# Optimization experiments

Measured on AMD Instinct MI355X. Metric: run time of the kernel, lower is better.

The kernel has to match this reference:

```python
import jax, jax.numpy as jnp
import numpy as np

N, E, DIN, DOUT, DE = 100000, 250000, 32, 32, 13


def setup_inputs() -> dict:
    key = jax.random.key(0)
    ks = jax.random.split(key, 10)
    def u(k, shape, fan):
        b = 1.0 / np.sqrt(fan)
        return jax.random.uniform(k, shape, jnp.float32, -b, b)
    x = jax.random.normal(ks[0], (N, DIN), jnp.float32)
    edge_index = jax.random.randint(ks[1], (2, E), 0, N)
    edge_attr = jax.random.uniform(ks[2], (E, DE), jnp.float32)
    # NNConv's edge network: Linear(DE -> DIN*DOUT)
    nn_w = u(ks[3], (DIN * DOUT, DE), DE)
    nn_b = u(ks[4], (DIN * DOUT,), DE)
    # NNConv root weight + bias
    root = u(ks[5], (DIN, DOUT), DIN)
    bias = jnp.zeros((DOUT,), jnp.float32)
    # GRU(input=DIN, hidden=DOUT), single layer, seq_len=1
    w_ih = u(ks[6], (3 * DOUT, DIN), DOUT)
    w_hh = u(ks[7], (3 * DOUT, DOUT), DOUT)
    b_ih = u(ks[8], (3 * DOUT,), DOUT)
    b_hh = u(ks[9], (3 * DOUT,), DOUT)
    return dict(x=x, edge_attr=edge_attr, nn_w=nn_w, nn_b=nn_b, root=root,
                bias=bias, w_ih=w_ih, w_hh=w_hh, b_ih=b_ih, b_hh=b_hh,
                edge_index=edge_index)


def reference(x, edge_attr, nn_w, nn_b, root, bias, w_ih, w_hh, b_ih, b_hh, edge_index):
    identity = x
    h0 = x  # h is None -> h = x.unsqueeze(0); squeeze the seq dim here
    # norm='_None' (identity) and Dropout in eval mode (identity)
    src, dst = edge_index[0], edge_index[1]
    # NNConv: per-edge weight matrix from edge_attr  [E, DIN, DOUT]
    W = (edge_attr @ nn_w.T + nn_b).reshape(E, DIN, DOUT)
    msg = jnp.einsum('ei,eio->eo', x[src], W)           # [E, DOUT]
    agg = jax.ops.segment_sum(msg, dst, num_segments=N)  # [N, DOUT]
    cnt = jax.ops.segment_sum(jnp.ones((E, 1), x.dtype), dst, num_segments=N)
    mean = agg / jnp.maximum(cnt, 1.0)                   # aggr='mean'
    conv = mean + x @ root + bias
    # celu then GRU step (seq_len=1)
    c = jax.nn.celu(conv)
    gi = c @ w_ih.T + b_ih
    gh = h0 @ w_hh.T + b_hh
    ir, iz, ic = jnp.split(gi, 3, axis=1)
    hr, hz, hc = jnp.split(gh, 3, axis=1)
    r = jax.nn.sigmoid(ir + hr)
    z = jax.nn.sigmoid(iz + hz)
    n = jnp.tanh(ic + r * hc)
    h_new = (1.0 - z) * n + z * h0
    out = jax.nn.relu(h_new + identity)  # res=True, act=ReLU
    return out, h_new[None]
```

## Files before the change

### kernel.cpp

```cpp
#include <hip/hip_runtime.h>
#include <hip/hip_bf16.h>
#include <stdint.h>

#define DIN 32
#define DOUT 32
#define DE 13

typedef float f32x4 __attribute__((ext_vector_type(4)));
typedef short s16x8 __attribute__((ext_vector_type(8)));
typedef int   i32x4 __attribute__((ext_vector_type(4)));
typedef unsigned int u32x4 __attribute__((ext_vector_type(4)));

__device__ __forceinline__ float bf2f(unsigned short u) {
    return __uint_as_float(((uint32_t)u) << 16);
}
__device__ __forceinline__ unsigned short f2bf(float f) {
    uint32_t b = __float_as_uint(f);
    b += 0x7FFFu + ((b >> 16) & 1u);
    return (unsigned short)(b >> 16);
}
__device__ __forceinline__ uint32_t pk2(float a, float b) {
    float2 t; t.x = a; t.y = b;
    __hip_bfloat162 h = __float22bfloat162_rn(t);
    return *(uint32_t*)&h;
}
__device__ __forceinline__ float sigm(float v) { return 1.f / (1.f + __expf(-v)); }
__device__ __forceinline__ float tanh_fast(float v) { return 2.f / (1.f + __expf(-2.f * v)) - 1.f; }


__global__ __launch_bounds__(256) void kH(const int* __restrict__ ei,
                                          int* __restrict__ cntI, int E) {
    int e = blockIdx.x * 256 + threadIdx.x;
    if (e < E) atomicAdd(&cntI[ei[E + e]], 1);
}

__global__ __launch_bounds__(1024) void kA(const int* __restrict__ cntI,
        int* __restrict__ base, float* __restrict__ degF,
        unsigned int* __restrict__ gtot, int N) {
    __shared__ int wsum[16];
    __shared__ unsigned int bbase;
    const int tid = threadIdx.x;
    const int lane = tid & 63;
    const int wv = tid >> 6;
    const int n = blockIdx.x * 1024 + tid;
    int d = (n < N) ? cntI[n] : 0;
    int sc = d;
    #pragma unroll
    for (int o = 1; o < 64; o <<= 1) {
        int t = __shfl_up(sc, o, 64);
        if (lane >= o) sc += t;
    }
    if (lane == 63) wsum[wv] = sc;
    __syncthreads();
    if (tid == 0) {
        int tot = 0;
        #pragma unroll
        for (int w = 0; w < 16; ++w) { int t = wsum[w]; wsum[w] = tot; tot += t; }
        bbase = atomicAdd(gtot, (unsigned int)tot);
    }
    __syncthreads();
    if (n < N) {
        base[n] = (int)bbase + wsum[wv] + (sc - d);
        degF[n] = (float)d;
    }
}

#define KE_LDS (28 * 512)
__global__ __launch_bounds__(256, 4) void kE(const float* __restrict__ x,
        const float* __restrict__ ea, const int* __restrict__ ei,
        const float* __restrict__ nn_w, const float* __restrict__ nn_b,
        uint32_t* __restrict__ msg, const int* __restrict__ base,
        int* __restrict__ cntI, int E) {
    __shared__ unsigned short Al[KE_LDS];
    __shared__ uint32_t trD[4][2][256];
    const int tid = threadIdx.x;
    for (int t = tid; t < KE_LDS; t += 256) {
        int j = t & 7;
        int lane = (t >> 3) & 63;
        int tile = t >> 9;
        int at2 = tile >= 14 ? 1 : 0;
        int kt = tile - at2 * 14;
        int o = at2 * 16 + (lane & 15);
        int i = ((lane >> 4) << 3) + j;
        float v = (kt < 13) ? nn_w[(i * 32 + o) * 13 + kt] : nn_b[i * 32 + o];
        Al[t] = f2bf(v);
    }
    __syncthreads();
    const int lane = tid & 63;
    const int wv = tid >> 6;
    const int el = lane & 15;
    const int quad = lane >> 4;
    const int q8 = quad << 3;
    const int wave = (blockIdx.x * 256 + tid) >> 6;
    const int nw = (gridDim.x * 256) >> 6;
    const int nstrips = E >> 4;
    int sC = wave;
    if (sC >= nstrips) return;
    int sN = sC + nw, sNN = sN + nw;

    const int eC = (sC << 4) + el;
    const int srcC = ei[eC];
    const int dstC = ei[E + eC];
    int srcN = 0, dstN = 0;
    if (sN < nstrips) {
        const int e1 = (sN << 4) + el;
        srcN = ei[e1];
        dstN = ei[E + e1];
    }
    {
        const float* eab = ea + (size_t)(sC << 4) * 13;
        #pragma unroll
        for (int t = 0; t < 4; ++t) {
            int idx = t * 64 + lane;
            if (idx < 208) trD[wv][0][idx] = __float_as_uint(eab[idx]);
        }
    }
    uint32_t eaR[4] = {0u, 0u, 0u, 0u};
    if (sN < nstrips) {
        const float* eab = ea + (size_t)(sN << 4) * 13;
        #pragma unroll
        for (int t = 0; t < 4; ++t) {
            int idx = t * 64 + lane;
            eaR[t] = (idx < 208) ? __float_as_uint(eab[idx]) : 0u;
        }
    }
    const float* xq0 = x + (size_t)srcC * 32 + q8;
    f32x4 xlo = *(const f32x4*)xq0;
    f32x4 xhi = *(const f32x4*)(xq0 + 4);
    int posC = 0;
    if (lane < 16)
        posC = base[dstC] + atomicSub(&cntI[dstC], 1) - 1;

    int pb = 0;
    const f32x4 zz = {0.f, 0.f, 0.f, 0.f};
    for (;;) {
        const bool hasN  = sN  < nstrips;
        const bool hasNN = sNN < nstrips;
        int srcNN = 0, dstNN = 0;
        if (hasNN) {
            const int e2 = (sNN << 4) + el;
            srcNN = ei[e2];
            dstNN = ei[E + e2];
        }
        if (hasN) {
            #pragma unroll
            for (int t = 0; t < 4; ++t) {
                int idx = t * 64 + lane;
                if (idx < 208) trD[wv][pb ^ 1][idx] = eaR[t];
            }
        }
        if (hasNN) {
            const float* eab = ea + (size_t)(sNN << 4) * 13;
            #pragma unroll
            for (int t = 0; t < 4; ++t) {
                int idx = t * 64 + lane;
                eaR[t] = (idx < 208) ? __float_as_uint(eab[idx]) : 0u;
            }
        }
        int posN = 0;
        if (hasN && lane < 16)
            posN = base[dstN] + atomicSub(&cntI[dstN], 1) - 1;
        i32x4 bi;
        bi[0] = pk2(xlo[0], xlo[1]);
        bi[1] = pk2(xlo[2], xlo[3]);
        bi[2] = pk2(xhi[0], xhi[1]);
        bi[3] = pk2(xhi[2], xhi[3]);
        s16x8 bfr = __builtin_bit_cast(s16x8, bi);
        s16x8 aB0 = *(const s16x8*)&Al[13 * 512 + lane * 8];
        s16x8 aB1 = *(const s16x8*)&Al[27 * 512 + lane * 8];
        f32x4 acc0 = __builtin_amdgcn_mfma_f32_16x16x32_bf16(aB0, bfr, zz, 0, 0, 0);
        f32x4 acc1 = __builtin_amdgcn_mfma_f32_16x16x32_bf16(aB1, bfr, zz, 0, 0, 0);
        #pragma unroll
        for (int kt = 0; kt < 13; ++kt) {
            s16x8 a0 = *(const s16x8*)&Al[kt * 512 + lane * 8];
            s16x8 a1 = *(const s16x8*)&Al[(14 + kt) * 512 + lane * 8];
            f32x4 y0 = __builtin_amdgcn_mfma_f32_16x16x32_bf16(a0, bfr, zz, 0, 0, 0);
            f32x4 y1 = __builtin_amdgcn_mfma_f32_16x16x32_bf16(a1, bfr, zz, 0, 0, 0);
            float gk = __uint_as_float(trD[wv][pb][el * 13 + kt]);
            #pragma unroll
            for (int r = 0; r < 4; ++r) {
                acc0[r] = fmaf(gk, y0[r], acc0[r]);
                acc1[r] = fmaf(gk, y1[r], acc1[r]);
            }
        }
        {
            u32x4 pw;
            pw[0] = pk2(acc0[0], acc1[0]);
            pw[1] = pk2(acc0[1], acc1[1]);
            pw[2] = pk2(acc0[2], acc1[2]);
            pw[3] = pk2(acc0[3], acc1[3]);
            *(u32x4*)&trD[wv][pb][el * 16 + quad * 4] = pw;
        }
        uint32_t v4s[4];
        int pp[4];
        #pragma unroll
        for (int p = 0; p < 4; ++p) {
            int e4 = (p << 2) + quad;
            v4s[p] = trD[wv][pb][e4 * 16 + el];
            pp[p] = __shfl(posC, e4, 64);
        }
        if (hasN) {
            const float* xq = x + (size_t)srcN * 32 + q8;
            xlo = *(const f32x4*)xq;
            xhi = *(const f32x4*)(xq + 4);
        }
        __builtin_amdgcn_sched_barrier(0);
        #pragma unroll
        for (int p = 0; p < 4; ++p)
            msg[(size_t)pp[p] * 16 + el] = v4s[p];
        __builtin_amdgcn_sched_barrier(0);
        if (!hasN) break;
        sC = sN; sN = sNN; sNN += nw;
        srcN = srcNN; dstN = dstNN;
        posC = posN;
        pb ^= 1;
    }
}

__global__ __launch_bounds__(256, 4) void kF(const float* __restrict__ x,
        const uint32_t* __restrict__ msg, const int* __restrict__ base,
        const float* __restrict__ degF,
        const float* __restrict__ root, const float* __restrict__ bias,
        const float* __restrict__ w_ih, const float* __restrict__ w_hh,
        const float* __restrict__ b_ih, const float* __restrict__ b_hh,
        float* __restrict__ out, float* __restrict__ hnew, int N) {
    __shared__ __align__(16) char smem[30720];
    unsigned short* Bl = (unsigned short*)smem;
    float* scr = (float*)(smem + 14336);
    unsigned short* clds = (unsigned short*)(smem + 14336);
    const int tid = threadIdx.x;
    {
        *(f32x4*)&scr[tid * 4] = *(const f32x4*)&root[tid * 4];
        #pragma unroll
        for (int it = 0; it < 3; ++it)
            *(f32x4*)&scr[1024 + it * 1024 + tid * 4] =
                *(const f32x4*)&w_hh[it * 1024 + tid * 4];
    }
    __syncthreads();
    for (int t = tid; t < 8 * 512; t += 256) {
        int j = t & 7;
        int ln = (t >> 3) & 63;
        int tt = t >> 9;
        int i = ((ln >> 4) << 3) + j;
        int c = ln & 15;
        int col = tt * 16 + c;
        float v = (col < 32) ? scr[i * 32 + col] : scr[1024 + (col - 32) * 32 + i];
        Bl[t] = f2bf(v);
    }
    __syncthreads();
    #pragma unroll
    for (int it = 0; it < 3; ++it)
        *(f32x4*)&scr[it * 1024 + tid * 4] = *(const f32x4*)&w_ih[it * 1024 + tid * 4];
    __syncthreads();
    for (int t = tid + 8 * 512; t < 14 * 512; t += 256) {
        int j = t & 7;
        int ln = (t >> 3) & 63;
        int tt = t >> 9;
        int i = ((ln >> 4) << 3) + j;
        int c = ln & 15;
        Bl[t] = f2bf(scr[((tt - 8) * 16 + c) * 32 + i]);
    }
    __syncthreads();
    const int lane = tid & 63;
    const int wv = tid >> 6;
    const int c15 = lane & 15;
    const int rowb = (lane >> 4) << 2;
    unsigned short* cl = clds + wv * 512;
    float binit[14];
    #pragma unroll
    for (int t = 0; t < 2; ++t) binit[t] = bias[t * 16 + c15];
    #pragma unroll
    for (int t = 2; t < 8; ++t) binit[t] = b_hh[t * 16 + c15 - 32];
    #pragma unroll
    for (int u = 0; u < 6; ++u) binit[8 + u] = b_ih[u * 16 + c15];
    int wave = (blockIdx.x * 256 + tid) >> 6;
    const int nw = (gridDim.x * 256) >> 6;
    const int nstrips = N >> 4;
    for (int s = wave; s < nstrips; s += nw) {
        const int n0 = s << 4;
        const float* xp = x + (size_t)(n0 + c15) * 32 + ((lane >> 4) << 3);
        f32x4 x0 = *(const f32x4*)xp;
        f32x4 x1 = *(const f32x4*)(xp + 4);
        int bs[4]; float dg[4]; float xr[4][2], ag[4][2];
        #pragma unroll
        for (int r = 0; r < 4; ++r) {
            const int n = n0 + rowb + r;
            bs[r] = base[n];
            dg[r] = degF[n];
            xr[r][0] = x[(size_t)n * 32 + c15];
            xr[r][1] = x[(size_t)n * 32 + 16 + c15];
        }
        #pragma unroll
        for (int r = 0; r < 4; ++r) {
            float a0 = 0.f, a1 = 0.f;
            const int dgi = (int)dg[r];
            const uint32_t* mp = msg + (size_t)bs[r] * 16 + c15;
            for (int j = 0; j < dgi; ++j) {
                uint32_t w = mp[j * 16];
                a0 += bf2f((unsigned short)(w & 0xFFFFu));
                a1 += bf2f((unsigned short)(w >> 16));
            }
            ag[r][0] = a0; ag[r][1] = a1;
        }
        s16x8 a;
        a[0] = (short)f2bf(x0[0]); a[1] = (short)f2bf(x0[1]);
        a[2] = (short)f2bf(x0[2]); a[3] = (short)f2bf(x0[3]);
        a[4] = (short)f2bf(x1[0]); a[5] = (short)f2bf(x1[1]);
        a[6] = (short)f2bf(x1[2]); a[7] = (short)f2bf(x1[3]);
        f32x4 D[8];
        #pragma unroll
        for (int t = 0; t < 8; ++t) {
            s16x8 b = *(const s16x8*)&Bl[(t * 64 + lane) * 8];
            f32x4 ci = {binit[t], binit[t], binit[t], binit[t]};
            D[t] = __builtin_amdgcn_mfma_f32_16x16x32_bf16(a, b, ci, 0, 0, 0);
        }
        #pragma unroll
        for (int r = 0; r < 4; ++r) {
            float icn = 1.f / fmaxf(dg[r], 1.f);
            #pragma unroll
            for (int t = 0; t < 2; ++t) {
                float conv = ag[r][t] * icn + D[t][r];
                float cv = conv > 0.f ? conv : (__expf(conv) - 1.f);
                cl[(rowb + r) * 32 + t * 16 + c15] = f2bf(cv);
            }
        }
        s16x8 a2 = *(const s16x8*)&cl[c15 * 32 + ((lane >> 4) << 3)];
        f32x4 G[6];
        #pragma unroll
        for (int u = 0; u < 6; ++u) {
            s16x8 b = *(const s16x8*)&Bl[((8 + u) * 64 + lane) * 8];
            f32x4 ci = {binit[8 + u], binit[8 + u], binit[8 + u], binit[8 + u]};
            G[u] = __builtin_amdgcn_mfma_f32_16x16x32_bf16(a2, b, ci, 0, 0, 0);
        }
        #pragma unroll
        for (int t = 0; t < 2; ++t) {
            #pragma unroll
            for (int r = 0; r < 4; ++r) {
                float rg = sigm(G[t][r] + D[2 + t][r]);
                float z  = sigm(G[2 + t][r] + D[4 + t][r]);
                float nn = tanh_fast(G[4 + t][r] + rg * D[6 + t][r]);
                float h  = (1.f - z) * nn + z * xr[r][t];
                float ov = h + xr[r][t];
                size_t oi = (size_t)(n0 + rowb + r) * 32 + t * 16 + c15;
                out[oi]  = ov > 0.f ? ov : 0.f;
                hnew[oi] = h;
            }
        }
    }
}

extern "C" void kernel_launch(void* const* d_in, const int* in_sizes, int n_in,
                              void* d_out, int out_size, void* d_ws, size_t ws_size,
                              hipStream_t stream) {
    const float* x    = (const float*)d_in[0];
    const float* ea   = (const float*)d_in[1];
    const float* nn_w = (const float*)d_in[2];
    const float* nn_b = (const float*)d_in[3];
    const float* root = (const float*)d_in[4];
    const float* bias = (const float*)d_in[5];
    const float* w_ih = (const float*)d_in[6];
    const float* w_hh = (const float*)d_in[7];
    const float* b_ih = (const float*)d_in[8];
    const float* b_hh = (const float*)d_in[9];
    const int*   ei   = (const int*)d_in[10];
    const int N = in_sizes[0] / DIN;
    const int E = in_sizes[10] / 2;
    float* out  = (float*)d_out;
    float* hnew = out + (size_t)N * DOUT;

    uint32_t* msg  = (uint32_t*)d_ws;
    char* p1 = (char*)d_ws + (size_t)E * 64;
    int*   base = (int*)p1;
    float* degF = (float*)(p1 + (size_t)N * 4);
    int*   cntI = (int*)(p1 + (size_t)N * 8);
    unsigned int* gtot = (unsigned int*)(p1 + (size_t)N * 12);

    hipMemsetAsync(cntI, 0, (size_t)N * 4 + 4, stream);
    kH<<<(E + 255) / 256, 256, 0, stream>>>(ei, cntI, E);
    kA<<<(N + 1023) / 1024, 1024, 0, stream>>>(cntI, base, degF, gtot, N);
    kE<<<1024, 256, 0, stream>>>(x, ea, ei, nn_w, nn_b, msg, base, cntI, E);
    kF<<<1024, 256, 0, stream>>>(x, msg, base, degF, root, bias,
                                 w_ih, w_hh, b_ih, b_hh, out, hnew, N);
}
```

Before: 171.2 us.

## Enlarge edge-kernel blocks and interleave per-row message gathers in node kernel

The edge kernel now runs 1024-thread blocks (512 blocks) instead of 256-thread blocks, so the 28KB bf16 weight tile in LDS is built once per 16 waves rather than per 4, cutting redundant global loads and conversion work. The node kernel's aggregation loop now walks all four rows together up to the maximum degree with predicated loads, giving more independent memory requests in flight. The x loads for the residual are also deferred until after the MFMAs. The trade-offs are extra wasted loads for low-degree rows, a larger LDS footprint per block that may limit occupancy, and higher register pressure from the interleaved gather.

```diff
diff --git a/kernel.cpp b/kernel.cpp
--- a/kernel.cpp
+++ b/kernel.cpp
@@ -66,15 +66,15 @@
 }
 
 #define KE_LDS (28 * 512)
-__global__ __launch_bounds__(256, 4) void kE(const float* __restrict__ x,
+__global__ __launch_bounds__(1024, 8) void kE(const float* __restrict__ x,
         const float* __restrict__ ea, const int* __restrict__ ei,
         const float* __restrict__ nn_w, const float* __restrict__ nn_b,
         uint32_t* __restrict__ msg, const int* __restrict__ base,
         int* __restrict__ cntI, int E) {
     __shared__ unsigned short Al[KE_LDS];
-    __shared__ uint32_t trD[4][2][256];
+    __shared__ uint32_t trD[16][2][256];
     const int tid = threadIdx.x;
-    for (int t = tid; t < KE_LDS; t += 256) {
+    for (int t = tid; t < KE_LDS; t += 1024) {
         int j = t & 7;
         int lane = (t >> 3) & 63;
         int tile = t >> 9;
@@ -91,8 +91,8 @@
     const int el = lane & 15;
     const int quad = lane >> 4;
     const int q8 = quad << 3;
-    const int wave = (blockIdx.x * 256 + tid) >> 6;
-    const int nw = (gridDim.x * 256) >> 6;
+    const int wave = (blockIdx.x * 1024 + tid) >> 6;
+    const int nw = (gridDim.x * 1024) >> 6;
     const int nstrips = E >> 4;
     int sC = wave;
     if (sC >= nstrips) return;
@@ -278,30 +278,31 @@
     const int nstrips = N >> 4;
     for (int s = wave; s < nstrips; s += nw) {
         const int n0 = s << 4;
-        const float* xp = x + (size_t)(n0 + c15) * 32 + ((lane >> 4) << 3);
-        f32x4 x0 = *(const f32x4*)xp;
-        f32x4 x1 = *(const f32x4*)(xp + 4);
-        int bs[4]; float dg[4]; float xr[4][2], ag[4][2];
+        int bs[4]; float dg[4]; int di[4];
         #pragma unroll
         for (int r = 0; r < 4; ++r) {
             const int n = n0 + rowb + r;
             bs[r] = base[n];
             dg[r] = degF[n];
-            xr[r][0] = x[(size_t)n * 32 + c15];
-            xr[r][1] = x[(size_t)n * 32 + 16 + c15];
-        }
-        #pragma unroll
-        for (int r = 0; r < 4; ++r) {
-            float a0 = 0.f, a1 = 0.f;
-            const int dgi = (int)dg[r];
-            const uint32_t* mp = msg + (size_t)bs[r] * 16 + c15;
-            for (int j = 0; j < dgi; ++j) {
-                uint32_t w = mp[j * 16];
-                a0 += bf2f((unsigned short)(w & 0xFFFFu));
-                a1 += bf2f((unsigned short)(w >> 16));
-            }
-            ag[r][0] = a0; ag[r][1] = a1;
-        }
+            di[r] = (int)dg[r];
+        }
+        int dmax = di[0];
+        #pragma unroll
+        for (int r = 1; r < 4; ++r) dmax = di[r] > dmax ? di[r] : dmax;
+        float a0[4] = {0.f, 0.f, 0.f, 0.f}, a1[4] = {0.f, 0.f, 0.f, 0.f};
+        for (int j = 0; j < dmax; ++j) {
+            #pragma unroll
+            for (int r = 0; r < 4; ++r) {
+                int jj = j < di[r] ? j : 0;
+                uint32_t w = msg[(size_t)(bs[r] + jj) * 16 + c15];
+                bool p = j < di[r];
+                a0[r] += p ? bf2f((unsigned short)(w & 0xFFFFu)) : 0.f;
+                a1[r] += p ? bf2f((unsigned short)(w >> 16)) : 0.f;
+            }
+        }
+        const float* xp = x + (size_t)(n0 + c15) * 32 + ((lane >> 4) << 3);
+        f32x4 x0 = *(const f32x4*)xp;
+        f32x4 x1 = *(const f32x4*)(xp + 4);
         s16x8 a;
         a[0] = (short)f2bf(x0[0]); a[1] = (short)f2bf(x0[1]);
         a[2] = (short)f2bf(x0[2]); a[3] = (short)f2bf(x0[3]);
@@ -317,12 +318,12 @@
         #pragma unroll
         for (int r = 0; r < 4; ++r) {
             float icn = 1.f / fmaxf(dg[r], 1.f);
-            #pragma unroll
-            for (int t = 0; t < 2; ++t) {
-                float conv = ag[r][t] * icn + D[t][r];
-                float cv = conv > 0.f ? conv : (__expf(conv) - 1.f);
-                cl[(rowb + r) * 32 + t * 16 + c15] = f2bf(cv);
-            }
+            float conv0 = a0[r] * icn + D[0][r];
+            float conv1 = a1[r] * icn + D[1][r];
+            float cv0 = conv0 > 0.f ? conv0 : (__expf(conv0) - 1.f);
+            float cv1 = conv1 > 0.f ? conv1 : (__expf(conv1) - 1.f);
+            cl[(rowb + r) * 32 + c15] = f2bf(cv0);
+            cl[(rowb + r) * 32 + 16 + c15] = f2bf(cv1);
         }
         s16x8 a2 = *(const s16x8*)&cl[c15 * 32 + ((lane >> 4) << 3)];
         f32x4 G[6];
@@ -331,6 +332,13 @@
             s16x8 b = *(const s16x8*)&Bl[((8 + u) * 64 + lane) * 8];
             f32x4 ci = {binit[8 + u], binit[8 + u], binit[8 + u], binit[8 + u]};
             G[u] = __builtin_amdgcn_mfma_f32_16x16x32_bf16(a2, b, ci, 0, 0, 0);
+        }
+        float xr[4][2];
+        #pragma unroll
+        for (int r = 0; r < 4; ++r) {
+            const int n = n0 + rowb + r;
+            xr[r][0] = x[(size_t)n * 32 + c15];
+            xr[r][1] = x[(size_t)n * 32 + 16 + c15];
         }
         #pragma unroll
         for (int t = 0; t < 2; ++t) {
@@ -378,7 +386,7 @@
     hipMemsetAsync(cntI, 0, (size_t)N * 4 + 4, stream);
     kH<<<(E + 255) / 256, 256, 0, stream>>>(ei, cntI, E);
     kA<<<(N + 1023) / 1024, 1024, 0, stream>>>(cntI, base, degF, gtot, N);
-    kE<<<1024, 256, 0, stream>>>(x, ea, ei, nn_w, nn_b, msg, base, cntI, E);
+    kE<<<512, 1024, 0, stream>>>(x, ea, ei, nn_w, nn_b, msg, base, cntI, E);
     kF<<<1024, 256, 0, stream>>>(x, msg, base, degF, root, bias,
                                  w_ih, w_hh, b_ih, b_hh, out, hnew, N);
 }
```

After: 172.9 us. No clear change (+1.0%).
